# Performance work log

Hardware: AMD Instinct MI355X
Metric: run time of the kernel (lower is better)

## Reference

```python
import jax, jax.numpy as jnp
import numpy as np

NEG_SLOPE = 0.2  # PyG GATv2Conv default negative_slope
EPS = 1e-16      # PyG softmax denominator eps


def _gatv2_conv(x, src, dst, Wl, bl, Wr, br, att, bias, heads, out_ch):
    """PyG GATv2Conv (share_weights=False, concat=True, self-loops already in edges)."""
    N = x.shape[0]
    xl = (x @ Wl + bl).reshape(N, heads, out_ch)  # values / source transform
    xr = (x @ Wr + br).reshape(N, heads, out_ch)  # target transform
    m = jax.nn.leaky_relu(xl[src] + xr[dst], NEG_SLOPE)      # [E,H,C]
    e = jnp.einsum('ehc,hc->eh', m, att)                      # [E,H]
    emax = jax.ops.segment_max(e, dst, num_segments=N)       # [N,H]
    ee = jnp.exp(e - emax[dst])
    denom = jax.ops.segment_sum(ee, dst, num_segments=N)
    alpha = ee / (denom[dst] + EPS)                           # scatter-softmax over dst
    out = jax.ops.segment_sum(xl[src] * alpha[:, :, None], dst, num_segments=N)
    return out.reshape(N, heads * out_ch) + bias


def setup_inputs() -> dict:
    key = jax.random.key(0)
    ks = jax.random.split(key, 16)
    N, E, DIN, DH, H, DOUT = 50000, 800000, 128, 16, 8, 64
    x = jax.random.normal(ks[0], (N, DIN), dtype=jnp.float32)
    edge_index = jax.random.randint(ks[1], (2, E), 0, N, dtype=jnp.int64)
    g = lambda k, shape: jax.random.normal(k, shape, dtype=jnp.float32) * (1.0 / np.sqrt(shape[0]))
    params = {
        'Wl1': g(ks[2], (DIN, H * DH)), 'bl1': jnp.zeros((H * DH,), jnp.float32),
        'Wr1': g(ks[3], (DIN, H * DH)), 'br1': jnp.zeros((H * DH,), jnp.float32),
        'att1': g(ks[4], (H, DH)), 'bias1': jnp.zeros((H * DH,), jnp.float32),
        'Wl2': g(ks[5], (H * DH, DOUT)), 'bl2': jnp.zeros((DOUT,), jnp.float32),
        'Wr2': g(ks[6], (H * DH, DOUT)), 'br2': jnp.zeros((DOUT,), jnp.float32),
        'att2': g(ks[7], (1, DOUT)), 'bias2': jnp.zeros((DOUT,), jnp.float32),
    }
    return {'x': x, 'edge_index': edge_index, **params}


def reference(x, edge_index, Wl1, bl1, Wr1, br1, att1, bias1,
              Wl2, bl2, Wr2, br2, att2, bias2):
    N = x.shape[0]
    loop = jnp.arange(N, dtype=edge_index.dtype)
    ei = jnp.concatenate([edge_index, jnp.stack([loop, loop])], axis=1)  # add self-loops
    src, dst = ei[0], ei[1]
    # eval mode: F.dropout is identity (p=0.6 dropouts skipped)
    h = _gatv2_conv(x, src, dst, Wl1, bl1, Wr1, br1, att1, bias1, heads=8, out_ch=16)
    h = jax.nn.elu(h)
    h = _gatv2_conv(h, src, dst, Wl2, bl2, Wr2, br2, att2, bias2, heads=1, out_ch=64)
    out = jax.nn.log_softmax(h, axis=1)
    predictions = jnp.argmax(out, axis=1)
    return (h, out, predictions)
```

## Files before the change

kernel.cpp:

```cpp
#include <hip/hip_runtime.h>
#include <hip/hip_bf16.h>

typedef unsigned short u16;
typedef __attribute__((ext_vector_type(8))) short bf8v;
typedef __attribute__((ext_vector_type(4))) float f4v;

#define N_NODES 50000
#define N_EDGES 800000
#define ET (N_EDGES + N_NODES)
#define D1 128
#define D2 64
#define NEG 0.2f
#define EPSF 1e-16f
#define NTILES_PAD 3128
#define NP (NTILES_PAD * 16)

#define O_XL1    0
#define O_XR1    6400000
#define O_AH     12800000
#define O_AM     16003072
#define O_AL     19206144
#define O_B1H    22409216
#define O_B1M    22425600
#define O_B1L    22441984
#define O_B2H    22458368
#define O_B2M    22466560
#define O_B2L    22474752
#define O_WF     22482944
#define O_SRC    22483968
#define O_DST    22908968
#define O_DEG    23333968
#define O_ROWPTR 23383968
#define O_RANK   23433969
#define O_CSR    23858969
#define O_FLAGS  24283969
#define O_PART   24283971
#define O_HIST   24284167
#define O_BCUR   24284423
#define O_PERM   24284679

#define W_BL1   0
#define W_BR1   128
#define W_ATT1  256
#define W_BIAS1 384
#define W_BL2   512
#define W_BR2   576
#define W_ATT2  640
#define W_BIAS2 704

#define NB_SCAN  196
#define NB_CVT   3321
#define NB_PACKX 3128
#define NB_PREP  (NB_CVT + NB_PACKX + 128 + 64 + 1)
#define NB_G1    3128
#define NB_SG    (NB_G1 + NB_CVT)

__device__ __forceinline__ float load_f32(const void* src, int i, int isbf16) {
    if (isbf16) {
        u16 u = ((const u16*)src)[i];
        return __uint_as_float((unsigned)u << 16);
    }
    return ((const float*)src)[i];
}
__device__ __forceinline__ u16 f2b(float v) {
    __hip_bfloat16 h = __float2bfloat16(v);
    return *(u16*)&h;
}
__device__ __forceinline__ float b2f(u16 u) { return __uint_as_float((unsigned)u << 16); }

__device__ __forceinline__ void split3(float v, u16& hi, u16& mid, u16& lo) {
    hi = f2b(v);
    float r1 = v - b2f(hi);
    mid = f2b(r1);
    float r2 = r1 - b2f(mid);
    lo = f2b(r2);
}

__global__ void init_k(int* deg, const u16* x16, const int* ei32, int* flags, int* hist) {
    int b = blockIdx.x;
    if (b < NB_SCAN) {
        int i = b * 256 + threadIdx.x;
        if (i < N_NODES) deg[i] = 0;
        return;
    }
    if (b == NB_SCAN + 1) {
        hist[threadIdx.x] = 0;
        return;
    }
    int lane = threadIdx.x;
    if (lane >= 64) return;
    int hits = 0;
    for (int j = lane; j < 32768; j += 64) {
        u16 u = x16[2 * j];
        if (((u >> 7) & 0xFF) == 0xFF) hits++;
    }
#pragma unroll
    for (int off = 32; off > 0; off >>= 1) hits += __shfl_xor(hits, off);
    int nz = 0;
    if (lane < 32) nz = ei32[2 * lane + 1];
#pragma unroll
    for (int off = 32; off > 0; off >>= 1) nz |= __shfl_xor(nz, off);
    if (lane == 0) { flags[0] = hits ? 0 : 1; flags[1] = nz ? 0 : 1; }
}

__global__ void prep_k(const int* __restrict__ ei,
                       u16* __restrict__ srcA, u16* __restrict__ dstA,
                       u16* __restrict__ rank, int* __restrict__ deg,
                       const void* x, u16* AH, u16* AM, u16* AL,
                       const void* Wl1, const void* Wr1, u16* B1H, u16* B1M, u16* B1L,
                       const void* Wl2, const void* Wr2, u16* B2H, u16* B2M, u16* B2L,
                       const void* bl1, const void* br1, const void* att1, const void* bias1,
                       const void* bl2, const void* br2, const void* att2, const void* bias2,
                       float* Wf, const int* flags) {
    int b = blockIdx.x, t = threadIdx.x;
    int fb = flags[0];
    if (b < NB_CVT) {
        int e = b * 256 + t;
        if (e < ET) {
            int s, d;
            if (e < N_EDGES) {
                if (flags[1]) { s = ei[2 * e]; d = ei[2 * (N_EDGES + e)]; }
                else          { s = ei[e];     d = ei[N_EDGES + e]; }
            } else {
                s = d = e - N_EDGES;
            }
            srcA[e] = (u16)s; dstA[e] = (u16)d;
            rank[e] = (u16)atomicAdd(&deg[d], 1);
        }
        return;
    }
    b -= NB_CVT;
    if (b < NB_PACKX) {
        int i = b * 256 + t;
        int j = i * 8;
        int tile = j >> 11;
        int jj = j & 2047;
        int r = tile * 16 + ((jj >> 3) & 15);
        int k0 = (jj >> 7) * 8;
        uint4 H = {0, 0, 0, 0}, M = {0, 0, 0, 0}, L = {0, 0, 0, 0};
        u16* Hp = (u16*)&H; u16* Mp = (u16*)&M; u16* Lp = (u16*)&L;
        if (r < N_NODES) {
            if (fb) {
                H = *(const uint4*)((const u16*)x + r * D1 + k0);
            } else {
                float4 xa = *(const float4*)((const float*)x + r * D1 + k0);
                float4 xb = *(const float4*)((const float*)x + r * D1 + k0 + 4);
                float vv[8] = {xa.x, xa.y, xa.z, xa.w, xb.x, xb.y, xb.z, xb.w};
#pragma unroll
                for (int e2 = 0; e2 < 8; e2++) split3(vv[e2], Hp[e2], Mp[e2], Lp[e2]);
            }
        }
        *(uint4*)(AH + j) = H;
        *(uint4*)(AM + j) = M;
        *(uint4*)(AL + j) = L;
        return;
    }
    b -= NB_PACKX;
    if (b < 128) {
        int i = b * 256 + t;
        int k = i >> 8, n = i & 255;
        float v = (n < 128) ? load_f32(Wl1, k * 128 + n, fb)
                            : load_f32(Wr1, k * 128 + (n - 128), fb);
        u16 hi, mid, lo; split3(v, hi, mid, lo);
        int idx = ((k >> 3) * 256 + n) * 8 + (k & 7);
        B1H[idx] = hi; B1M[idx] = mid; B1L[idx] = lo;
        return;
    }
    b -= 128;
    if (b < 64) {
        int i = b * 256 + t;
        int k = i >> 7, n = i & 127;
        float v = (n < 64) ? load_f32(Wl2, k * 64 + n, fb)
                           : load_f32(Wr2, k * 64 + (n - 64), fb);
        u16 hi, mid, lo; split3(v, hi, mid, lo);
        int idx = ((k >> 3) * 128 + n) * 8 + (k & 7);
        B2H[idx] = hi; B2M[idx] = mid; B2L[idx] = lo;
        return;
    }
    if (t < 128) {
        Wf[W_BL1 + t]   = load_f32(bl1, t, fb);
        Wf[W_BR1 + t]   = load_f32(br1, t, fb);
        Wf[W_ATT1 + t]  = load_f32(att1, t, fb);
        Wf[W_BIAS1 + t] = load_f32(bias1, t, fb);
        if (t < 64) {
            Wf[W_BL2 + t]   = load_f32(bl2, t, fb);
            Wf[W_BR2 + t]   = load_f32(br2, t, fb);
            Wf[W_ATT2 + t]  = load_f32(att2, t, fb);
            Wf[W_BIAS2 + t] = load_f32(bias2, t, fb);
        }
    }
}

__global__ __launch_bounds__(256) void sa_k(const int* __restrict__ deg, int* __restrict__ part,
                                            int* __restrict__ hist) {
    int b = blockIdx.x, t = threadIdx.x;
    if (b < NB_SCAN) {
        __shared__ int s[256];
        int i = b * 256 + t;
        s[t] = (i < N_NODES) ? deg[i] : 0;
        __syncthreads();
        for (int off = 128; off > 0; off >>= 1) {
            if (t < off) s[t] += s[t + off];
            __syncthreads();
        }
        if (t == 0) part[b] = s[0];
        return;
    }
    __shared__ int lh[256];
    lh[t] = 0;
    __syncthreads();
    int i = (b - NB_SCAN) * 256 + t;
    if (i < N_NODES) atomicAdd(&lh[min(deg[i], 255)], 1);
    __syncthreads();
    if (lh[t]) atomicAdd(&hist[t], lh[t]);
}

__global__ __launch_bounds__(256) void sb_k(int* __restrict__ part, const int* __restrict__ hist,
                                            int* __restrict__ bcur) {
    __shared__ int s[256];
    int t = threadIdx.x;
    if (blockIdx.x == 0) {
        s[t] = (t < NB_SCAN) ? part[t] : 0;
        __syncthreads();
        for (int off = 1; off < 256; off <<= 1) {
            int v = (t >= off) ? s[t - off] : 0;
            __syncthreads();
            s[t] += v;
            __syncthreads();
        }
        if (t < NB_SCAN) part[t] = (t == 0) ? 0 : s[t - 1];
        return;
    }
    int h = hist[t];
    s[t] = h;
    __syncthreads();
    for (int off = 1; off < 256; off <<= 1) {
        int v = (t >= off) ? s[t - off] : 0;
        __syncthreads();
        s[t] += v;
        __syncthreads();
    }
    bcur[t] = s[t] - h;
}

__global__ __launch_bounds__(256) void sc_k(const int* __restrict__ deg, const int* __restrict__ part,
                                            int* __restrict__ rowptr,
                                            int* __restrict__ bcur, int* __restrict__ perm) {
    int b = blockIdx.x, t = threadIdx.x;
    if (b < NB_SCAN) {
        __shared__ int s[256];
        int i = b * 256 + t;
        int v = (i < N_NODES) ? deg[i] : 0;
        s[t] = v;
        __syncthreads();
        for (int off = 1; off < 256; off <<= 1) {
            int u = (t >= off) ? s[t - off] : 0;
            __syncthreads();
            s[t] += u;
            __syncthreads();
        }
        int excl = part[b] + s[t] - v;
        if (i < N_NODES) rowptr[i] = excl;
        if (i == N_NODES - 1) rowptr[N_NODES] = excl + v;
        return;
    }
    __shared__ int lh[256];
    __shared__ int lbase[256];
    lh[t] = 0;
    __syncthreads();
    int i = (b - NB_SCAN) * 256 + t;
    int bk = -1, myrank = 0;
    if (i < N_NODES) {
        bk = min(deg[i], 255);
        myrank = atomicAdd(&lh[bk], 1);
    }
    __syncthreads();
    if (lh[t]) lbase[t] = atomicAdd(&bcur[t], lh[t]);
    __syncthreads();
    if (bk >= 0) perm[lbase[bk] + myrank] = i;
}

#define MFMA6(acc, ah, am, al, bh, bm, bl)                                    \
    acc = __builtin_amdgcn_mfma_f32_16x16x32_bf16(ah, bl, acc, 0, 0, 0);      \
    acc = __builtin_amdgcn_mfma_f32_16x16x32_bf16(am, bm, acc, 0, 0, 0);      \
    acc = __builtin_amdgcn_mfma_f32_16x16x32_bf16(al, bh, acc, 0, 0, 0);      \
    acc = __builtin_amdgcn_mfma_f32_16x16x32_bf16(ah, bm, acc, 0, 0, 0);      \
    acc = __builtin_amdgcn_mfma_f32_16x16x32_bf16(am, bh, acc, 0, 0, 0);      \
    acc = __builtin_amdgcn_mfma_f32_16x16x32_bf16(ah, bh, acc, 0, 0, 0);

__global__ __launch_bounds__(256) void sg_k(const u16* __restrict__ AH, const u16* __restrict__ AM,
                                            const u16* __restrict__ AL,
                                            const u16* __restrict__ BH, const u16* __restrict__ BM,
                                            const u16* __restrict__ BL,
                                            const float* __restrict__ Wf,
                                            float* __restrict__ xl, float* __restrict__ xr,
                                            const u16* __restrict__ srcA, const u16* __restrict__ dstA,
                                            const u16* __restrict__ rank, const int* __restrict__ rowptr,
                                            u16* __restrict__ csr) {
    int b = blockIdx.x;
    if (b < NB_G1) {
        int w = threadIdx.x >> 6, l = threadIdx.x & 63;
        int tile = (b >> 2) * 4 + w;
        int cb = (b & 3) << 6;
        int lr = l & 15, lg = l >> 4;
        f4v acc[4];
#pragma unroll
        for (int nt = 0; nt < 4; nt++) acc[nt] = (f4v)(0.f);
        int aoff = tile * 2048 + lg * 128 + lr * 8;
#pragma unroll
        for (int ks = 0; ks < 4; ks++) {
            bf8v ah = *(const bf8v*)(AH + aoff + ks * 512);
            bf8v am = *(const bf8v*)(AM + aoff + ks * 512);
            bf8v al = *(const bf8v*)(AL + aoff + ks * 512);
            int boff = ((ks * 4 + lg) * 256 + cb + lr) * 8;
#pragma unroll
            for (int nt = 0; nt < 4; nt++) {
                bf8v bh = *(const bf8v*)(BH + boff + nt * 128);
                bf8v bm = *(const bf8v*)(BM + boff + nt * 128);
                bf8v bl = *(const bf8v*)(BL + boff + nt * 128);
                MFMA6(acc[nt], ah, am, al, bh, bm, bl)
            }
        }
        int r0 = tile * 16 + lg * 4;
        if (r0 >= N_NODES) return;
#pragma unroll
        for (int nt = 0; nt < 4; nt++) {
            int col = cb + nt * 16 + lr;
            float bias = (col < D1) ? Wf[W_BL1 + col] : Wf[W_BR1 + col - D1];
            float* dst = (col < D1) ? (xl + col) : (xr + col - D1);
#pragma unroll
            for (int j = 0; j < 4; j++) {
                int row = r0 + j;
                dst[(size_t)row * D1] = acc[nt][j] + bias;
            }
        }
        return;
    }
    int e = (b - NB_G1) * 256 + threadIdx.x;
    if (e < ET) {
        int d = dstA[e];
        csr[rowptr[d] + rank[e]] = srcA[e];
    }
}

union bfu { bf8v v; u16 s[8]; };
__global__ __launch_bounds__(256) void gemm2_mfma(const float* __restrict__ hA,
                                                  const u16* __restrict__ BH, const u16* __restrict__ BM,
                                                  const u16* __restrict__ BL,
                                                  const float* __restrict__ Wf,
                                                  float* __restrict__ xl2, float* __restrict__ xr2) {
    int w = threadIdx.x >> 6, l = threadIdx.x & 63;
    int tile = blockIdx.x * 4 + w;
    int cb = blockIdx.y << 6;
    int lr = l & 15, lg = l >> 4;
    int r = tile * 16 + lr;
    int rc = min(r, N_NODES - 1);
    f4v acc[4];
#pragma unroll
    for (int nt = 0; nt < 4; nt++) acc[nt] = (f4v)(0.f);
#pragma unroll
    for (int ks = 0; ks < 4; ks++) {
        const float* hp = hA + (size_t)rc * D1 + ks * 32 + lg * 8;
        float4 p0 = *(const float4*)hp;
        float4 p1 = *(const float4*)(hp + 4);
        float vv[8] = {p0.x, p0.y, p0.z, p0.w, p1.x, p1.y, p1.z, p1.w};
        bfu ah, am, al;
#pragma unroll
        for (int j = 0; j < 8; j++) split3(vv[j], ah.s[j], am.s[j], al.s[j]);
        int boff = ((ks * 4 + lg) * 128 + cb + lr) * 8;
#pragma unroll
        for (int nt = 0; nt < 4; nt++) {
            bf8v bh = *(const bf8v*)(BH + boff + nt * 128);
            bf8v bm = *(const bf8v*)(BM + boff + nt * 128);
            bf8v bl = *(const bf8v*)(BL + boff + nt * 128);
            MFMA6(acc[nt], ah.v, am.v, al.v, bh, bm, bl)
        }
    }
    int r0 = tile * 16 + lg * 4;
    if (r0 >= N_NODES) return;
#pragma unroll
    for (int nt = 0; nt < 4; nt++) {
        int col = cb + nt * 16 + lr;
        float bias = (col < D2) ? Wf[W_BL2 + col] : Wf[W_BR2 + col - D2];
        float* dst = (col < D2) ? (xl2 + col) : (xr2 + col - D2);
#pragma unroll
        for (int j = 0; j < 4; j++) {
            int row = r0 + j;
            dst[(size_t)row * D2] = acc[nt][j] + bias;
        }
    }
}

#define L1STEP(a)                                                              \
    {                                                                          \
        float m0 = a.x + xr4.x; m0 = fmaxf(m0, NEG * m0);                      \
        float m1 = a.y + xr4.y; m1 = fmaxf(m1, NEG * m1);                      \
        float m2 = a.z + xr4.z; m2 = fmaxf(m2, NEG * m2);                      \
        float m3 = a.w + xr4.w; m3 = fmaxf(m3, NEG * m3);                      \
        float p = m0 * at4.x + m1 * at4.y + m2 * at4.z + m3 * at4.w;           \
        p += __shfl_xor(p, 1);                                                 \
        p += __shfl_xor(p, 2);                                                 \
        p = fminf(fmaxf(p, -60.f), 60.f);                                      \
        float wgt = __expf(p);                                                 \
        l += wgt;                                                              \
        acc.x = fmaf(wgt, a.x, acc.x);                                         \
        acc.y = fmaf(wgt, a.y, acc.y);                                         \
        acc.z = fmaf(wgt, a.z, acc.z);                                         \
        acc.w = fmaf(wgt, a.w, acc.w);                                         \
    }

__global__ __launch_bounds__(256) void l1_agg(const int* __restrict__ rowptr, const u16* __restrict__ csr,
                                              const int* __restrict__ perm,
                                              const float* __restrict__ xl, const float* __restrict__ xr,
                                              const float* __restrict__ Wf, float* __restrict__ hbuf) {
    int n = perm[(blockIdx.x * 256 + threadIdx.x) >> 5];
    int q = threadIdx.x & 31;
    const float4* xl4 = (const float4*)xl;
    float4 xr4 = ((const float4*)(xr + (size_t)n * D1))[q];
    float4 at4 = ((const float4*)(Wf + W_ATT1))[q];
    int i0 = rowptr[n], i1 = rowptr[n + 1];
    float l = 0.f;
    float4 acc = {0.f, 0.f, 0.f, 0.f};
    float4 a = xl4[(size_t)csr[i0] * 32 + q];
    for (int i = i0 + 1; i < i1; i++) {
        float4 an = xl4[(size_t)csr[i] * 32 + q];
        L1STEP(a)
        a = an;
    }
    L1STEP(a)
    float rinv = 1.f / l;
    float4 bi4 = ((const float4*)(Wf + W_BIAS1))[q];
    float v0 = acc.x * rinv + bi4.x; v0 = v0 > 0.f ? v0 : expm1f(v0);
    float v1 = acc.y * rinv + bi4.y; v1 = v1 > 0.f ? v1 : expm1f(v1);
    float v2 = acc.z * rinv + bi4.z; v2 = v2 > 0.f ? v2 : expm1f(v2);
    float v3 = acc.w * rinv + bi4.w; v3 = v3 > 0.f ? v3 : expm1f(v3);
    float4 hv = {v0, v1, v2, v3};
    ((float4*)(hbuf + (size_t)n * D1))[q] = hv;
}

#define L2STEP(a)                                                              \
    {                                                                          \
        float m0 = a.x + xr4.x; m0 = fmaxf(m0, NEG * m0);                      \
        float m1 = a.y + xr4.y; m1 = fmaxf(m1, NEG * m1);                      \
        float m2 = a.z + xr4.z; m2 = fmaxf(m2, NEG * m2);                      \
        float m3 = a.w + xr4.w; m3 = fmaxf(m3, NEG * m3);                      \
        float p = m0 * at4.x + m1 * at4.y + m2 * at4.z + m3 * at4.w;           \
        p += __shfl_xor(p, 1);                                                 \
        p += __shfl_xor(p, 2);                                                 \
        p += __shfl_xor(p, 4);                                                 \
        p += __shfl_xor(p, 8);                                                 \
        p = fminf(fmaxf(p, -80.f), 80.f);                                      \
        float wgt = __expf(p);                                                 \
        l += wgt;                                                              \
        acc.x = fmaf(wgt, a.x, acc.x);                                         \
        acc.y = fmaf(wgt, a.y, acc.y);                                         \
        acc.z = fmaf(wgt, a.z, acc.z);                                         \
        acc.w = fmaf(wgt, a.w, acc.w);                                         \
    }

__global__ __launch_bounds__(256) void l2_agg(const int* __restrict__ rowptr, const u16* __restrict__ csr,
                                              const int* __restrict__ perm,
                                              const float* __restrict__ xl, const float* __restrict__ xr,
                                              const float* __restrict__ Wf, float* __restrict__ out) {
    int n = perm[(blockIdx.x * 256 + threadIdx.x) >> 4];
    int q = threadIdx.x & 15;
    const float4* xl4 = (const float4*)xl;
    float4 xr4 = ((const float4*)(xr + (size_t)n * D2))[q];
    float4 at4 = ((const float4*)(Wf + W_ATT2))[q];
    int i0 = rowptr[n], i1 = rowptr[n + 1];
    float l = 0.f;
    float4 acc = {0.f, 0.f, 0.f, 0.f};
    float4 a = xl4[(size_t)csr[i0] * 16 + q];
    for (int i = i0 + 1; i < i1; i++) {
        float4 an = xl4[(size_t)csr[i] * 16 + q];
        L2STEP(a)
        a = an;
    }
    L2STEP(a)
    float rinv = 1.f / (l + EPSF);
    float4 bi4 = ((const float4*)(Wf + W_BIAS2))[q];
    float v0 = acc.x * rinv + bi4.x;
    float v1 = acc.y * rinv + bi4.y;
    float v2 = acc.z * rinv + bi4.z;
    float v3 = acc.w * rinv + bi4.w;
    float4 hv = {v0, v1, v2, v3};
    ((float4*)(out + (size_t)n * D2))[q] = hv;
    float mx = fmaxf(fmaxf(v0, v1), fmaxf(v2, v3));
#pragma unroll
    for (int off = 1; off < 16; off <<= 1) mx = fmaxf(mx, __shfl_xor(mx, off));
    float sum = expf(v0 - mx) + expf(v1 - mx) + expf(v2 - mx) + expf(v3 - mx);
#pragma unroll
    for (int off = 1; off < 16; off <<= 1) sum += __shfl_xor(sum, off);
    float lse = mx + logf(sum);
    float4 ls = {v0 - lse, v1 - lse, v2 - lse, v3 - lse};
    ((float4*)(out + (size_t)N_NODES * D2 + (size_t)n * D2))[q] = ls;
    float bv = v0; int bi = 4 * q;
    if (v1 > bv) { bv = v1; bi = 4 * q + 1; }
    if (v2 > bv) { bv = v2; bi = 4 * q + 2; }
    if (v3 > bv) { bv = v3; bi = 4 * q + 3; }
#pragma unroll
    for (int off = 1; off < 16; off <<= 1) {
        float ov = __shfl_xor(bv, off);
        int   oi = __shfl_xor(bi, off);
        if (ov > bv || (ov == bv && oi < bi)) { bv = ov; bi = oi; }
    }
    if (q == 0) out[(size_t)2 * N_NODES * D2 + n] = (float)bi;
}

extern "C" void kernel_launch(void* const* d_in, const int* in_sizes, int n_in,
                              void* d_out, int out_size, void* d_ws, size_t ws_size,
                              hipStream_t stream) {
    const void* x  = d_in[0];
    const int*  ei = (const int*)d_in[1];

    float* ws = (float*)d_ws;
    float* xl1    = ws + O_XL1;
    float* xr1    = ws + O_XR1;
    u16*   AH     = (u16*)(ws + O_AH);
    u16*   AM     = (u16*)(ws + O_AM);
    u16*   AL     = (u16*)(ws + O_AL);
    float* hbuf   = ws + O_AH;
    u16*   B1H    = (u16*)(ws + O_B1H);
    u16*   B1M    = (u16*)(ws + O_B1M);
    u16*   B1L    = (u16*)(ws + O_B1L);
    u16*   B2H    = (u16*)(ws + O_B2H);
    u16*   B2M    = (u16*)(ws + O_B2M);
    u16*   B2L    = (u16*)(ws + O_B2L);
    float* Wf     = ws + O_WF;
    u16*   srcA   = (u16*)(ws + O_SRC);
    u16*   dstA   = (u16*)(ws + O_DST);
    int*   deg    = (int*)(ws + O_DEG);
    int*   rowptr = (int*)(ws + O_ROWPTR);
    u16*   rank   = (u16*)(ws + O_RANK);
    u16*   csr    = (u16*)(ws + O_CSR);
    int*   flags  = (int*)(ws + O_FLAGS);
    int*   part   = (int*)(ws + O_PART);
    int*   hist   = (int*)(ws + O_HIST);
    int*   bcur   = (int*)(ws + O_BCUR);
    int*   perm   = (int*)(ws + O_PERM);

    float* xl2 = xl1;
    float* xr2 = xl1 + 3200000;

    init_k<<<NB_SCAN + 2, 256, 0, stream>>>(deg, (const u16*)x, ei, flags, hist);
    prep_k<<<NB_PREP, 256, 0, stream>>>(ei, srcA, dstA, rank, deg,
                                        x, AH, AM, AL,
                                        d_in[2], d_in[4], B1H, B1M, B1L,
                                        d_in[8], d_in[10], B2H, B2M, B2L,
                                        d_in[3], d_in[5], d_in[6], d_in[7],
                                        d_in[9], d_in[11], d_in[12], d_in[13],
                                        Wf, flags);
    sa_k<<<2 * NB_SCAN, 256, 0, stream>>>(deg, part, hist);
    sb_k<<<2, 256, 0, stream>>>(part, hist, bcur);
    sc_k<<<2 * NB_SCAN, 256, 0, stream>>>(deg, part, rowptr, bcur, perm);
    sg_k<<<NB_SG, 256, 0, stream>>>(AH, AM, AL, B1H, B1M, B1L, Wf, xl1, xr1,
                                    srcA, dstA, rank, rowptr, csr);

    l1_agg<<<6250, 256, 0, stream>>>(rowptr, csr, perm, xl1, xr1, Wf, hbuf);
    gemm2_mfma<<<dim3(NTILES_PAD / 4, 2), 256, 0, stream>>>(hbuf, B2H, B2M, B2L, Wf, xl2, xr2);
    l2_agg<<<3125, 256, 0, stream>>>(rowptr, csr, perm, xl2, xr2, Wf, (float*)d_out);
}
```

Baseline: 256.3 us.

## Deepen gather prefetch, use exp2 with prescaled attention, split init into memsets

Both aggregation kernels now prefetch two neighbor rows ahead instead of one, so more gather latency is hidden. The attention vector is prescaled by log2(e), so the softmax weight comes from exp2f with a single med3 clamp instead of __expf plus fmin/fmax. The combined init kernel is replaced by two hipMemsetAsync calls and a one-wave detect kernel. The extra launches and the higher register use from deeper prefetch may offset some of the gain.

```diff
diff --git a/kernel.cpp b/kernel.cpp
--- a/kernel.cpp
+++ b/kernel.cpp
@@ -12,6 +12,7 @@
 #define D2 64
 #define NEG 0.2f
 #define EPSF 1e-16f
+#define LOG2E 1.44269504f
 #define NTILES_PAD 3128
 #define NP (NTILES_PAD * 16)
 
@@ -76,19 +77,8 @@
     lo = f2b(r2);
 }
 
-__global__ void init_k(int* deg, const u16* x16, const int* ei32, int* flags, int* hist) {
-    int b = blockIdx.x;
-    if (b < NB_SCAN) {
-        int i = b * 256 + threadIdx.x;
-        if (i < N_NODES) deg[i] = 0;
-        return;
-    }
-    if (b == NB_SCAN + 1) {
-        hist[threadIdx.x] = 0;
-        return;
-    }
+__global__ __launch_bounds__(64) void detect_k(const u16* x16, const int* ei32, int* flags) {
     int lane = threadIdx.x;
-    if (lane >= 64) return;
     int hits = 0;
     for (int j = lane; j < 32768; j += 64) {
         u16 u = x16[2 * j];
@@ -400,8 +390,8 @@
         float p = m0 * at4.x + m1 * at4.y + m2 * at4.z + m3 * at4.w;           \
         p += __shfl_xor(p, 1);                                                 \
         p += __shfl_xor(p, 2);                                                 \
-        p = fminf(fmaxf(p, -60.f), 60.f);                                      \
-        float wgt = __expf(p);                                                 \
+        p = __builtin_amdgcn_fmed3f(p, -86.f, 86.f);                           \
+        float wgt = exp2f(p);                                                  \
         l += wgt;                                                              \
         acc.x = fmaf(wgt, a.x, acc.x);                                         \
         acc.y = fmaf(wgt, a.y, acc.y);                                         \
@@ -418,16 +408,22 @@
     const float4* xl4 = (const float4*)xl;
     float4 xr4 = ((const float4*)(xr + (size_t)n * D1))[q];
     float4 at4 = ((const float4*)(Wf + W_ATT1))[q];
+    at4.x *= LOG2E; at4.y *= LOG2E; at4.z *= LOG2E; at4.w *= LOG2E;
     int i0 = rowptr[n], i1 = rowptr[n + 1];
     float l = 0.f;
     float4 acc = {0.f, 0.f, 0.f, 0.f};
-    float4 a = xl4[(size_t)csr[i0] * 32 + q];
-    for (int i = i0 + 1; i < i1; i++) {
-        float4 an = xl4[(size_t)csr[i] * 32 + q];
-        L1STEP(a)
-        a = an;
-    }
-    L1STEP(a)
+    float4 a0 = xl4[(size_t)csr[i0] * 32 + q];
+    if (i0 + 1 < i1) {
+        float4 a1 = xl4[(size_t)csr[i0 + 1] * 32 + q];
+        for (int i = i0 + 2; i < i1; i++) {
+            float4 a2 = xl4[(size_t)csr[i] * 32 + q];
+            L1STEP(a0)
+            a0 = a1; a1 = a2;
+        }
+        L1STEP(a0)
+        a0 = a1;
+    }
+    L1STEP(a0)
     float rinv = 1.f / l;
     float4 bi4 = ((const float4*)(Wf + W_BIAS1))[q];
     float v0 = acc.x * rinv + bi4.x; v0 = v0 > 0.f ? v0 : expm1f(v0);
@@ -449,8 +445,8 @@
         p += __shfl_xor(p, 2);                                                 \
         p += __shfl_xor(p, 4);                                                 \
         p += __shfl_xor(p, 8);                                                 \
-        p = fminf(fmaxf(p, -80.f), 80.f);                                      \
-        float wgt = __expf(p);                                                 \
+        p = __builtin_amdgcn_fmed3f(p, -115.f, 115.f);                         \
+        float wgt = exp2f(p);                                                  \
         l += wgt;                                                              \
         acc.x = fmaf(wgt, a.x, acc.x);                                         \
         acc.y = fmaf(wgt, a.y, acc.y);                                         \
@@ -467,16 +463,22 @@
     const float4* xl4 = (const float4*)xl;
     float4 xr4 = ((const float4*)(xr + (size_t)n * D2))[q];
     float4 at4 = ((const float4*)(Wf + W_ATT2))[q];
+    at4.x *= LOG2E; at4.y *= LOG2E; at4.z *= LOG2E; at4.w *= LOG2E;
     int i0 = rowptr[n], i1 = rowptr[n + 1];
     float l = 0.f;
     float4 acc = {0.f, 0.f, 0.f, 0.f};
-    float4 a = xl4[(size_t)csr[i0] * 16 + q];
-    for (int i = i0 + 1; i < i1; i++) {
-        float4 an = xl4[(size_t)csr[i] * 16 + q];
-        L2STEP(a)
-        a = an;
-    }
-    L2STEP(a)
+    float4 a0 = xl4[(size_t)csr[i0] * 16 + q];
+    if (i0 + 1 < i1) {
+        float4 a1 = xl4[(size_t)csr[i0 + 1] * 16 + q];
+        for (int i = i0 + 2; i < i1; i++) {
+            float4 a2 = xl4[(size_t)csr[i] * 16 + q];
+            L2STEP(a0)
+            a0 = a1; a1 = a2;
+        }
+        L2STEP(a0)
+        a0 = a1;
+    }
+    L2STEP(a0)
     float rinv = 1.f / (l + EPSF);
     float4 bi4 = ((const float4*)(Wf + W_BIAS2))[q];
     float v0 = acc.x * rinv + bi4.x;
@@ -542,7 +544,9 @@
     float* xl2 = xl1;
     float* xr2 = xl1 + 3200000;
 
-    init_k<<<NB_SCAN + 2, 256, 0, stream>>>(deg, (const u16*)x, ei, flags, hist);
+    hipMemsetAsync(deg, 0, N_NODES * sizeof(int), stream);
+    hipMemsetAsync(hist, 0, 256 * sizeof(int), stream);
+    detect_k<<<1, 64, 0, stream>>>((const u16*)x, ei, flags);
     prep_k<<<NB_PREP, 256, 0, stream>>>(ei, srcA, dstA, rank, deg,
                                         x, AH, AM, AL,
                                         d_in[2], d_in[4], B1H, B1M, B1L,
```

Result: slower. 315.0 us (+22.9%).
